# Kernel tuning notes

Measured on AMD Instinct MI355X. Metric: run time of the kernel, lower is better.

Reference implementation:

```python
import jax, jax.numpy as jnp
import numpy as np
from functools import lru_cache


@lru_cache(maxsize=None)
def _mw_basis(L):
    """Fully-normalized associated Legendre basis on MW-style theta grid.

    Returns (Pfull, w):
      Pfull: (L, 2L-1, L) float32, Pfull[l, L-1+m, t] = Nbar_lm * P_l^m(cos theta_t)
             (zero for |m| > l), with Y_lm = Pfull * exp(i m phi).
      w:     (L,) float32 quadrature weights sin(theta)*dtheta*dphi.
    """
    t = np.arange(L)
    theta = np.pi * (2 * t + 1) / (2 * L - 1)  # MW theta samples
    ct, st = np.cos(theta), np.sin(theta)
    P = np.zeros((L, L, L))
    P[0, 0] = np.full(L, np.sqrt(1.0 / (4.0 * np.pi)))
    for m in range(1, L):
        P[m, m] = -np.sqrt((2.0 * m + 1.0) / (2.0 * m)) * st * P[m - 1, m - 1]
    for m in range(L - 1):
        P[m + 1, m] = np.sqrt(2.0 * m + 3.0) * ct * P[m, m]
    for m in range(L):
        for l in range(m + 2, L):
            a = np.sqrt((4.0 * l * l - 1.0) / (l * l - m * m))
            b = np.sqrt(((2.0 * l + 1.0) * (l - 1 - m) * (l - 1 + m)) / ((2.0 * l - 3.0) * (l * l - m * m)))
            P[l, m] = a * ct * P[l - 1, m] - b * P[l - 2, m]
    Pfull = np.zeros((L, 2 * L - 1, L), dtype=np.float32)
    for m in range(L):
        Pfull[:, L - 1 + m, :] = P[:, m, :]
        if m > 0:
            Pfull[:, L - 1 - m, :] = ((-1.0) ** m) * P[:, m, :]
    dang = 2.0 * np.pi / (2 * L - 1)  # theta and phi spacing
    w = (st * dang * dang).astype(np.float32)
    return jnp.asarray(Pfull), jnp.asarray(w)


def sht_forward(x):
    """x: (L, 2L-1, C) real -> flm: (L, 2L-1, C) complex, m indexed -(L-1)..(L-1)."""
    L = x.shape[0]
    P, w = _mw_basis(L)
    F = jnp.fft.fft(x.astype(jnp.complex64), axis=1)           # k = 0..2L-2
    F = jnp.concatenate([F[:, L:, :], F[:, :L, :]], axis=1)     # reorder to m = -(L-1)..L-1
    # flm = sum_t w_t Nbar P_l^m(theta_t) * Fm(theta_t)
    return jnp.einsum('lmt,tmc->lmc', P * w[None, None, :], F)


def sht_inverse(flm):
    """flm: (L, 2L-1, C) complex -> f: (L, 2L-1, C) complex on MW grid."""
    L = flm.shape[0]
    P, _ = _mw_basis(L)
    G = jnp.einsum('lmc,lmt->tmc', flm, P)                      # (theta, m, C)
    G = jnp.concatenate([G[:, L - 1:, :], G[:, :L - 1, :]], axis=1)  # m order -> fft k order
    return jnp.fft.ifft(G, axis=1) * (2 * L - 1)


def zero_pad_flm(flm, L_out):
    L_in = flm.shape[0]
    p = L_out - L_in
    return jnp.pad(flm, ((0, p), (p, p), (0, 0)))


L_IN = 256
L_FREQ = 128
L_OUT = 256
C_IN = 32
C_OUT = 32
T_DIM = 256


def setup_inputs() -> dict:
    key = jax.random.key(0)
    ks = jax.random.split(key, 8)
    return {
        'x': jax.random.normal(ks[0], (L_IN, 2 * L_IN - 1, C_IN), jnp.float32),
        't_emb': jax.random.normal(ks[1], (T_DIM,), jnp.float32),
        'weight_real': 0.02 * jax.random.normal(ks[2], (L_FREQ, C_IN, C_OUT), jnp.float32),
        'weight_imag': 0.02 * jax.random.normal(ks[3], (L_FREQ, C_IN, C_OUT), jnp.float32),
        'w_tr': jax.random.normal(ks[4], (T_DIM, L_FREQ), jnp.float32) / np.sqrt(T_DIM),
        'b_tr': jnp.zeros((L_FREQ,), jnp.float32),
        'w_ti': jax.random.normal(ks[5], (T_DIM, L_FREQ), jnp.float32) / np.sqrt(T_DIM),
        'b_ti': jnp.zeros((L_FREQ,), jnp.float32),
    }


def reference(x, t_emb, weight_real, weight_imag, w_tr, b_tr, w_ti, b_ti):
    # forward SHT over all channels at once
    flm = sht_forward(x)                                       # (L_in, 2L_in-1, C_in) complex64
    # bilinear resize of the spectrum to the used bandlimit (real/imag separately)
    tgt = (L_FREQ, 2 * L_FREQ - 1, flm.shape[2])
    flm = (jax.image.resize(jnp.real(flm), tgt, 'bilinear')
           + 1j * jax.image.resize(jnp.imag(flm), tgt, 'bilinear'))
    # time-modulated per-degree complex spectral weights
    t_cplx = (t_emb @ w_tr + b_tr) + 1j * (t_emb @ w_ti + b_ti)   # (L_freq,)
    weight = t_cplx[:, None, None] * (weight_real + 1j * weight_imag)  # (L_freq, C_in, C_out)
    flm = jnp.einsum('lmi,lio->lmo', flm, weight)
    # zero pad to output bandlimit and inverse SHT
    flm = zero_pad_flm(flm, L_OUT)                             # (L_out, 2L_out-1, C_out)
    x_out = jnp.real(sht_inverse(flm))
    return x_out
```

## Files before the change

### kernel.cpp

```cpp
#include <hip/hip_runtime.h>
#include <math.h>

#define PI_D 3.14159265358979323846

typedef short v8s __attribute__((ext_vector_type(8)));
typedef float v4f __attribute__((ext_vector_type(4)));

constexpr size_t OFF_PA   = 0;
constexpr size_t OFF_PT   = 8388608;
constexpr size_t OFF_SFRE = 12582912;
constexpr size_t OFF_SFIM = 14680064;
constexpr size_t OFF_FRE  = 16777216;
constexpr size_t OFF_FIM  = 18874368;
constexpr size_t OFF_CRE  = 20971520;
constexpr size_t OFF_CIM  = 22016000;
constexpr size_t OFF_AF   = 23060480;
constexpr size_t OFF_AI   = 23191552;
constexpr size_t OFF_WQ   = 23322624;
constexpr size_t OFF_TC   = 23322880;
constexpr size_t OFF_WLW  = 23323136;
constexpr size_t OFF_WLI  = 23323648;
constexpr size_t OFF_WMW  = 23324160;
constexpr size_t OFF_WMI  = 23325696;
constexpr size_t OFF_GRE  = OFF_FRE;
constexpr size_t OFF_GIM  = OFF_FIM;

__device__ __forceinline__ short f2bf(float f) {
  unsigned u = __float_as_uint(f);
  unsigned r = (u + 0x7FFFu + ((u >> 16) & 1u)) >> 16;
  return (short)r;
}

__global__ void k_prep(const float* t_emb, const float* w_tr, const float* b_tr,
                       const float* w_ti, const float* b_ti, float* ws) {
  int bx = blockIdx.x, tid = threadIdx.x;
  if (bx < 2048) {
    int g = bx * 256 + tid;
    bool inv = (g >= 262144);
    int gid = inv ? g - 262144 : g;
    int j = gid & 7, lane = (gid >> 3) & 63, ks = (gid >> 9) & 15, mt = gid >> 13;
    int m = mt * 16 + (lane & 15);
    int k = ks * 32 + ((lane >> 4) << 3) + j;
    float v = 0.f;
    if (!inv) {
      if (k < 511) {
        int mm = (m < 256) ? m : m - 256;
        int kk = (mm * k) % 511;
        float ang = (float)(2.0 * PI_D / 511.0) * (float)kk;
        float s, c; __sincosf(ang, &s, &c);
        v = (m < 256) ? c : -s;
      }
      ((short*)(ws + OFF_AF))[gid] = f2bf(v);
    } else {
      if (m < 511 && k < 510) {
        int jj = (k < 255) ? k : k - 255;
        int jm = jj - 127;
        int kk = ((jm * m) % 511 + 511) % 511;
        float ang = (float)(2.0 * PI_D / 511.0) * (float)kk;
        float s, c; __sincosf(ang, &s, &c);
        v = (k < 255) ? c : -s;
      }
      ((short*)(ws + OFF_AI))[gid] = f2bf(v);
    }
    return;
  }
  if (tid < 256) {
    double theta = PI_D * (2.0 * tid + 1.0) / 511.0;
    double dang = 2.0 * PI_D / 511.0;
    ws[OFF_WQ + tid] = (float)(sin(theta) * dang * dang);
  }
  {
    int h = tid >> 7, o = tid & 127;
    const float* W = h ? w_ti : w_tr;
    float s = h ? b_ti[o] : b_tr[o];
    for (int T = 0; T < 256; ++T) s += t_emb[T] * W[T * 128 + o];
    ws[OFF_TC + h * 128 + o] = s;
  }
  if (tid < 128) {
    double sf = 2.0 * tid + 0.5;
    double wv[4]; int iv[4]; double wsum = 0.0;
    for (int a = 0; a < 4; ++a) {
      int t = 2 * tid - 1 + a;
      double r = 1.0 - fabs(sf - (double)t) * 0.5;
      bool valid = (t >= 0 && t < 256 && r > 0.0);
      wv[a] = valid ? r : 0.0; iv[a] = valid ? t : 0;
      wsum += wv[a];
    }
    for (int a = 0; a < 4; ++a) {
      ws[OFF_WLW + tid * 4 + a] = (float)(wv[a] / wsum);
      ((int*)(ws + OFF_WLI))[tid * 4 + a] = iv[a];
    }
  }
  if (tid < 255) {
    double inv2 = 511.0 / 255.0;
    double sf = (tid + 0.5) * inv2 - 0.5;
    int t0 = (int)floor(sf) - 2;
    double wv[6]; int iv[6]; double wsum = 0.0;
    for (int b = 0; b < 6; ++b) {
      int t = t0 + b;
      double r = 1.0 - fabs(sf - (double)t) * (255.0 / 511.0);
      bool valid = (t >= 0 && t < 511 && r > 0.0);
      wv[b] = valid ? r : 0.0; iv[b] = valid ? t : 0;
      wsum += wv[b];
    }
    for (int b = 0; b < 6; ++b) {
      ws[OFF_WMW + tid * 6 + b] = (float)(wv[b] / wsum);
      ((int*)(ws + OFF_WMI))[tid * 6 + b] = iv[b];
    }
  }
}

__global__ __launch_bounds__(256) void k_legendre(float* ws) {
  int m = blockIdx.x, t = threadIdx.x;
  __shared__ double cA[256], cB[256], cS[256];
  {
    int l = t;
    if (l >= 1) cS[l] = -sqrt((2.0 * l + 1.0) / (2.0 * l));
    if (l >= m + 2) {
      double ll = l, mm = m;
      double den = ll * ll - mm * mm;
      cA[l] = sqrt((4.0 * ll * ll - 1.0) / den);
      cB[l] = sqrt((2.0 * ll + 1.0) * (ll - 1.0 - mm) * (ll - 1.0 + mm) /
                   ((2.0 * ll - 3.0) * den));
    }
  }
  __syncthreads();
  __shared__ short tile[16 * 280];
  __shared__ short tileT[256 * 34];
  bool wantPT = (m < 128);
  short* PAp = (short*)(ws + OFF_PA) + (size_t)m * 65536;
  short* PTp = (short*)(ws + OFF_PT) + (size_t)m * 65536;
  double theta = PI_D * (2.0 * t + 1.0) / 511.0;
  double ct = cos(theta), st = sin(theta);
  double p0 = sqrt(1.0 / (4.0 * PI_D));
  for (int k = 1; k <= m; ++k) p0 *= cS[k] * st;
  double pm1 = 0.0, pcur = 0.0;
  for (int lt = 0; lt < 16; ++lt) {
    for (int li = 0; li < 16; ++li) {
      int l = lt * 16 + li;
      float v;
      if (l < m) v = 0.f;
      else if (l == m) { pcur = p0; v = (float)pcur; }
      else if (l == m + 1) { pm1 = pcur; pcur = sqrt(2.0 * m + 3.0) * ct * pm1; v = (float)pcur; }
      else { double p2 = cA[l] * ct * pcur - cB[l] * pm1; pm1 = pcur; pcur = p2; v = (float)p2; }
      short bv = f2bf(v);
      tile[li * 280 + t] = bv;
      if (wantPT) tileT[t * 34 + li] = bv;
    }
    __syncthreads();
#pragma unroll
    for (int pass = 0; pass < 2; ++pass) {
      int ch = pass * 256 + t;
      int li = ch & 15, T0 = ch >> 4;
      size_t dst = (size_t)lt * 4096 + (size_t)(T0 >> 2) * 512 + (size_t)((T0 & 3) * 16 + li) * 8;
      *(v8s*)(PAp + dst) = *(const v8s*)(tile + li * 280 + T0 * 8);
    }
    if (wantPT) {
#pragma unroll
      for (int pass = 0; pass < 2; ++pass) {
        int ch = pass * 256 + t;
        int tt = ch >> 1, li0 = (ch & 1) * 8;
        size_t dst = (size_t)(tt >> 4) * 4096 + (size_t)(lt >> 1) * 512 +
                     (size_t)(((lt & 1) * 2 + (li0 >> 3)) * 16 + (tt & 15)) * 8;
        const int* src = (const int*)(tileT + tt * 34 + li0);
        int* d = (int*)(PTp + dst);
        d[0] = src[0]; d[1] = src[1]; d[2] = src[2]; d[3] = src[3];
      }
    }
    __syncthreads();
  }
}

__global__ __launch_bounds__(256) void k_gemm_f(const float* x, float* ws) {
  int nt = blockIdx.x, t = blockIdx.y;
  int tid = threadIdx.x, wave = tid >> 6, lane = tid & 63;
  const v8s* A = (const v8s*)(ws + OFF_AF);
  float wq = ws[OFF_WQ + t];
  const float* xb = x + (size_t)t * 511 * 32 + nt * 16 + (lane & 15);
  int phiB = (lane >> 4) << 3;
  int mtB = wave * 8;
  v4f acc[8];
#pragma unroll
  for (int i = 0; i < 8; ++i) acc[i] = (v4f){0.f, 0.f, 0.f, 0.f};
  for (int ks = 0; ks < 16; ++ks) {
    v8s b;
    int phi0 = ks * 32 + phiB;
#pragma unroll
    for (int j = 0; j < 8; ++j) {
      int phi = phi0 + j;
      float v = (phi < 511) ? wq * xb[(size_t)phi * 32] : 0.f;
      b[j] = f2bf(v);
    }
#pragma unroll
    for (int i = 0; i < 8; ++i) {
      v8s a = A[(size_t)((mtB + i) * 16 + ks) * 64 + lane];
      acc[i] = __builtin_amdgcn_mfma_f32_16x16x32_bf16(a, b, acc[i], 0, 0, 0);
    }
  }
  int quad = lane >> 4, cn = nt * 16 + (lane & 15);
#pragma unroll
  for (int i = 0; i < 8; ++i) {
    int mt = mtB + i;
#pragma unroll
    for (int r = 0; r < 4; ++r) {
      int mp = mt * 16 + quad * 4 + r;
      float v = acc[i][r];
      if (mp < 256) ws[OFF_FRE + ((size_t)mp * 256 + t) * 32 + cn] = v;
      else          ws[OFF_FIM + ((size_t)(mp - 256) * 256 + t) * 32 + cn] = v;
    }
  }
}

__global__ __launch_bounds__(512) void k_legfwd(float* ws) {
  int m = blockIdx.x;
  int tid = threadIdx.x, wave = tid >> 6, lane = tid & 63;
  const v8s* A = (const v8s*)(ws + OFF_PA) + (size_t)m * 8192;
  int mt0 = wave * 2;
  int cl = lane & 15, tB = (lane >> 4) << 3;
  v4f acc[2][4];
#pragma unroll
  for (int i = 0; i < 2; ++i)
#pragma unroll
    for (int n = 0; n < 4; ++n) acc[i][n] = (v4f){0.f, 0.f, 0.f, 0.f};
  bool sk0 = (mt0 * 16 + 15) < m;
  bool sk1 = (mt0 * 16 + 31) < m;
  if (!(sk0 && sk1)) {
    for (int ks = 0; ks < 8; ++ks) {
      int t0 = ks * 32 + tB;
      v8s b[4];
#pragma unroll
      for (int n = 0; n < 4; ++n) {
        int cp = n * 16 + cl;
        const float* Fb = ws + (cp < 32 ? OFF_FRE : OFF_FIM) +
                          (size_t)m * 8192 + (size_t)t0 * 32 + (cp & 31);
#pragma unroll
        for (int j = 0; j < 8; ++j) b[n][j] = f2bf(Fb[(size_t)j * 32]);
      }
      if (!sk0) {
        v8s a = A[(size_t)mt0 * 512 + ks * 64 + lane];
        acc[0][0] = __builtin_amdgcn_mfma_f32_16x16x32_bf16(a, b[0], acc[0][0], 0, 0, 0);
        acc[0][1] = __builtin_amdgcn_mfma_f32_16x16x32_bf16(a, b[1], acc[0][1], 0, 0, 0);
        acc[0][2] = __builtin_amdgcn_mfma_f32_16x16x32_bf16(a, b[2], acc[0][2], 0, 0, 0);
        acc[0][3] = __builtin_amdgcn_mfma_f32_16x16x32_bf16(a, b[3], acc[0][3], 0, 0, 0);
      }
      if (!sk1) {
        v8s a = A[(size_t)(mt0 + 1) * 512 + ks * 64 + lane];
        acc[1][0] = __builtin_amdgcn_mfma_f32_16x16x32_bf16(a, b[0], acc[1][0], 0, 0, 0);
        acc[1][1] = __builtin_amdgcn_mfma_f32_16x16x32_bf16(a, b[1], acc[1][1], 0, 0, 0);
        acc[1][2] = __builtin_amdgcn_mfma_f32_16x16x32_bf16(a, b[2], acc[1][2], 0, 0, 0);
        acc[1][3] = __builtin_amdgcn_mfma_f32_16x16x32_bf16(a, b[3], acc[1][3], 0, 0, 0);
      }
    }
  }
  int quad = lane >> 4;
#pragma unroll
  for (int i = 0; i < 2; ++i) {
    bool sk = i ? sk1 : sk0;
#pragma unroll
    for (int n = 0; n < 4; ++n) {
      int cp = n * 16 + cl;
      float* dst = ws + ((cp >= 32) ? OFF_SFIM : OFF_SFRE) + (size_t)m * 8192 + (cp & 31);
#pragma unroll
      for (int r = 0; r < 4; ++r) {
        int l = (mt0 + i) * 16 + quad * 4 + r;
        dst[(size_t)l * 32] = sk ? 0.f : acc[i][n][r];
      }
    }
  }
}

__global__ __launch_bounds__(256) void k_conv(const float* w_real, const float* w_imag, float* ws) {
  int jq = blockIdx.x, l = blockIdx.y;
  int tid = threadIdx.x;
  int jl = tid >> 5, o = tid & 31;
  __shared__ __align__(16) float wr[32 * 36];
  __shared__ __align__(16) float wi[32 * 36];
  __shared__ __align__(16) float fr[8 * 32];
  __shared__ __align__(16) float fi[8 * 32];
  {
    int oo = tid >> 3, i4 = (tid & 7) * 4;
    float tcr = ws[OFF_TC + l], tci = ws[OFF_TC + 128 + l];
#pragma unroll
    for (int q = 0; q < 4; ++q) {
      int i = i4 + q;
      float a = w_real[(size_t)l * 1024 + i * 32 + oo];
      float b = w_imag[(size_t)l * 1024 + i * 32 + oo];
      wr[oo * 36 + i] = tcr * a - tci * b;
      wi[oo * 36 + i] = tcr * b + tci * a;
    }
  }
  const float* SFRE = ws + OFF_SFRE;
  const float* SFIM = ws + OFF_SFIM;
  const float* WMW = ws + OFF_WMW;
  const int* WMI = (const int*)(ws + OFF_WMI);
  float wl[4]; int liv[4];
#pragma unroll
  for (int a = 0; a < 4; ++a) {
    wl[a] = ws[OFF_WLW + l * 4 + a];
    liv[a] = ((const int*)(ws + OFF_WLI))[l * 4 + a];
  }
  for (int ji = 0; ji < 8; ++ji) {
    int j = jq * 64 + ji * 8 + jl;
    int jp = (j < 255) ? j : 254;
    float accr = 0.f, acci = 0.f;
    for (int b = 0; b < 6; ++b) {
      float wm = WMW[jp * 6 + b];
      int jm = WMI[jp * 6 + b];
      bool mneg = (jm < 255);
      int mm = mneg ? (255 - jm) : (jm - 255);
      float fre_f = (mneg && (mm & 1)) ? -1.f : 1.f;
      float fim_f = mneg ? -fre_f : 1.f;
#pragma unroll
      for (int a = 0; a < 4; ++a) {
        float w = wm * wl[a];
        size_t base = ((size_t)mm * 256 + liv[a]) * 32 + o;
        accr = fmaf(w * fre_f, SFRE[base], accr);
        acci = fmaf(w * fim_f, SFIM[base], acci);
      }
    }
    __syncthreads();
    fr[jl * 32 + o] = accr;
    fi[jl * 32 + o] = acci;
    __syncthreads();
    float sr = 0.f, si = 0.f;
#pragma unroll
    for (int i0 = 0; i0 < 32; i0 += 4) {
      float4 f_r = *(const float4*)(fr + jl * 32 + i0);
      float4 f_i = *(const float4*)(fi + jl * 32 + i0);
      float4 w_r = *(const float4*)(wr + o * 36 + i0);
      float4 w_i = *(const float4*)(wi + o * 36 + i0);
      sr += f_r.x * w_r.x - f_i.x * w_i.x;  si += f_r.x * w_i.x + f_i.x * w_r.x;
      sr += f_r.y * w_r.y - f_i.y * w_i.y;  si += f_r.y * w_i.y + f_i.y * w_r.y;
      sr += f_r.z * w_r.z - f_i.z * w_i.z;  si += f_r.z * w_i.z + f_i.z * w_r.z;
      sr += f_r.w * w_r.w - f_i.w * w_i.w;  si += f_r.w * w_i.w + f_i.w * w_r.w;
    }
    if (j < 255) {
      float s = (j < 127 && ((127 - j) & 1)) ? -1.f : 1.f;
      ws[OFF_CRE + ((size_t)j * 128 + l) * 32 + o] = s * sr;
      ws[OFF_CIM + ((size_t)j * 128 + l) * 32 + o] = s * si;
    }
  }
}

__global__ __launch_bounds__(512) void k_gemm_linv(float* ws) {
  int j = blockIdx.x;
  int d = j - 127; int mm = (d < 0) ? -d : d;
  int tid = threadIdx.x, wave = tid >> 6, lane = tid & 63;
  const v8s* A = (const v8s*)(ws + OFF_PT) + (size_t)mm * 8192;
  int mt0 = wave * 2;
  int cl = lane & 15, lB = (lane >> 4) << 3;
  v4f acc[2][4];
#pragma unroll
  for (int i = 0; i < 2; ++i)
#pragma unroll
    for (int n = 0; n < 4; ++n) acc[i][n] = (v4f){0.f, 0.f, 0.f, 0.f};
  int ks0 = mm >> 5;
  for (int ks = ks0; ks < 4; ++ks) {
    int l0 = ks * 32 + lB;
    v8s b[4];
#pragma unroll
    for (int n = 0; n < 4; ++n) {
      int cp = n * 16 + cl;
      const float* Cb = ws + (cp < 32 ? OFF_CRE : OFF_CIM) +
                        ((size_t)j * 128 + l0) * 32 + (cp & 31);
#pragma unroll
      for (int j8 = 0; j8 < 8; ++j8) b[n][j8] = f2bf(Cb[(size_t)j8 * 32]);
    }
    v8s a0 = A[(size_t)mt0 * 512 + ks * 64 + lane];
    v8s a1 = A[(size_t)(mt0 + 1) * 512 + ks * 64 + lane];
    acc[0][0] = __builtin_amdgcn_mfma_f32_16x16x32_bf16(a0, b[0], acc[0][0], 0, 0, 0);
    acc[0][1] = __builtin_amdgcn_mfma_f32_16x16x32_bf16(a0, b[1], acc[0][1], 0, 0, 0);
    acc[0][2] = __builtin_amdgcn_mfma_f32_16x16x32_bf16(a0, b[2], acc[0][2], 0, 0, 0);
    acc[0][3] = __builtin_amdgcn_mfma_f32_16x16x32_bf16(a0, b[3], acc[0][3], 0, 0, 0);
    acc[1][0] = __builtin_amdgcn_mfma_f32_16x16x32_bf16(a1, b[0], acc[1][0], 0, 0, 0);
    acc[1][1] = __builtin_amdgcn_mfma_f32_16x16x32_bf16(a1, b[1], acc[1][1], 0, 0, 0);
    acc[1][2] = __builtin_amdgcn_mfma_f32_16x16x32_bf16(a1, b[2], acc[1][2], 0, 0, 0);
    acc[1][3] = __builtin_amdgcn_mfma_f32_16x16x32_bf16(a1, b[3], acc[1][3], 0, 0, 0);
  }
  int quad = lane >> 4;
#pragma unroll
  for (int i = 0; i < 2; ++i) {
#pragma unroll
    for (int n = 0; n < 4; ++n) {
      int cp = n * 16 + cl;
      float* dst = ws + ((cp >= 32) ? OFF_GIM : OFF_GRE) + (size_t)(cp & 31);
#pragma unroll
      for (int r = 0; r < 4; ++r) {
        int t = (mt0 + i) * 16 + quad * 4 + r;
        dst[((size_t)t * 255 + j) * 32] = acc[i][n][r];
      }
    }
  }
}

__global__ __launch_bounds__(256) void k_gemm_i(const float* ws, float* out) {
  int nt = blockIdx.x, t = blockIdx.y;
  int tid = threadIdx.x, wave = tid >> 6, lane = tid & 63;
  const v8s* A = (const v8s*)(ws + OFF_AI);
  const float* GRE = ws + OFF_GRE;
  const float* GIM = ws + OFF_GIM;
  int mtB = wave * 8;
  int cn = nt * 16 + (lane & 15);
  int kB = (lane >> 4) << 3;
  v4f acc[8];
#pragma unroll
  for (int i = 0; i < 8; ++i) acc[i] = (v4f){0.f, 0.f, 0.f, 0.f};
  for (int ks = 0; ks < 16; ++ks) {
    v8s b;
    int k0 = ks * 32 + kB;
#pragma unroll
    for (int j8 = 0; j8 < 8; ++j8) {
      int k = k0 + j8;
      float v = 0.f;
      if (k < 255)      v = GRE[((size_t)t * 255 + k) * 32 + cn];
      else if (k < 510) v = GIM[((size_t)t * 255 + (k - 255)) * 32 + cn];
      b[j8] = f2bf(v);
    }
#pragma unroll
    for (int i = 0; i < 8; ++i) {
      v8s a = A[(size_t)((mtB + i) * 16 + ks) * 64 + lane];
      acc[i] = __builtin_amdgcn_mfma_f32_16x16x32_bf16(a, b, acc[i], 0, 0, 0);
    }
  }
  int quad = lane >> 4;
#pragma unroll
  for (int i = 0; i < 8; ++i) {
    int mt = mtB + i;
#pragma unroll
    for (int r = 0; r < 4; ++r) {
      int phi = mt * 16 + quad * 4 + r;
      if (phi < 511) out[((size_t)t * 511 + phi) * 32 + cn] = acc[i][r];
    }
  }
}

extern "C" void kernel_launch(void* const* d_in, const int* in_sizes, int n_in,
                              void* d_out, int out_size, void* d_ws, size_t ws_size,
                              hipStream_t stream) {
  const float* x = (const float*)d_in[0];
  const float* t_emb = (const float*)d_in[1];
  const float* w_real = (const float*)d_in[2];
  const float* w_imag = (const float*)d_in[3];
  const float* w_tr = (const float*)d_in[4];
  const float* b_tr = (const float*)d_in[5];
  const float* w_ti = (const float*)d_in[6];
  const float* b_ti = (const float*)d_in[7];
  float* ws = (float*)d_ws;
  float* out = (float*)d_out;
  (void)in_sizes; (void)n_in; (void)out_size; (void)ws_size;

  hipLaunchKernelGGL(k_prep, dim3(2049), dim3(256), 0, stream,
                     t_emb, w_tr, b_tr, w_ti, b_ti, ws);
  hipLaunchKernelGGL(k_legendre, dim3(256), dim3(256), 0, stream, ws);
  hipLaunchKernelGGL(k_gemm_f, dim3(2, 256), dim3(256), 0, stream, x, ws);
  hipLaunchKernelGGL(k_legfwd, dim3(256), dim3(512), 0, stream, ws);
  hipLaunchKernelGGL(k_conv, dim3(4, 128), dim3(256), 0, stream, w_real, w_imag, ws);
  hipLaunchKernelGGL(k_gemm_linv, dim3(255), dim3(512), 0, stream, ws);
  hipLaunchKernelGGL(k_gemm_i, dim3(2, 256), dim3(256), 0, stream, ws, out);
}
```

Before: 230.0 us.

## Split GEMM tiles across more waves and register-prefetch B operands

The four MFMA GEMM kernels now give each wave fewer output tiles: the phi/k GEMMs use twice as many blocks, and the Legendre GEMMs use 1024-thread blocks with one M-tile per wave. Each kernel also software-pipelines the strided B-operand loads, reading the next k-slice into registers while MFMAs run on the current one. The aim is more parallelism and latency hiding for the global loads. In exchange, the shared B loads are repeated across more waves and blocks, and register pressure rises with 1024-thread blocks.

```diff
diff --git a/kernel.cpp b/kernel.cpp
--- a/kernel.cpp
+++ b/kernel.cpp
@@ -172,34 +172,49 @@
 }
 
 __global__ __launch_bounds__(256) void k_gemm_f(const float* x, float* ws) {
-  int nt = blockIdx.x, t = blockIdx.y;
+  int bx = blockIdx.x, t = blockIdx.y;
+  int nt = bx & 1, mh = bx >> 1;
   int tid = threadIdx.x, wave = tid >> 6, lane = tid & 63;
   const v8s* A = (const v8s*)(ws + OFF_AF);
   float wq = ws[OFF_WQ + t];
   const float* xb = x + (size_t)t * 511 * 32 + nt * 16 + (lane & 15);
   int phiB = (lane >> 4) << 3;
-  int mtB = wave * 8;
-  v4f acc[8];
-#pragma unroll
-  for (int i = 0; i < 8; ++i) acc[i] = (v4f){0.f, 0.f, 0.f, 0.f};
+  int mtB = mh * 16 + wave * 4;
+  v4f acc[4];
+#pragma unroll
+  for (int i = 0; i < 4; ++i) acc[i] = (v4f){0.f, 0.f, 0.f, 0.f};
+  float bv[8];
+#pragma unroll
+  for (int j = 0; j < 8; ++j) {
+    int phi = phiB + j;
+    bv[j] = (phi < 511) ? xb[(size_t)phi * 32] : 0.f;
+  }
   for (int ks = 0; ks < 16; ++ks) {
+    float bn[8];
+    if (ks < 15) {
+      int phi0 = (ks + 1) * 32 + phiB;
+#pragma unroll
+      for (int j = 0; j < 8; ++j) {
+        int phi = phi0 + j;
+        bn[j] = (phi < 511) ? xb[(size_t)phi * 32] : 0.f;
+      }
+    }
     v8s b;
-    int phi0 = ks * 32 + phiB;
-#pragma unroll
-    for (int j = 0; j < 8; ++j) {
-      int phi = phi0 + j;
-      float v = (phi < 511) ? wq * xb[(size_t)phi * 32] : 0.f;
-      b[j] = f2bf(v);
-    }
-#pragma unroll
-    for (int i = 0; i < 8; ++i) {
+#pragma unroll
+    for (int j = 0; j < 8; ++j) b[j] = f2bf(wq * bv[j]);
+#pragma unroll
+    for (int i = 0; i < 4; ++i) {
       v8s a = A[(size_t)((mtB + i) * 16 + ks) * 64 + lane];
       acc[i] = __builtin_amdgcn_mfma_f32_16x16x32_bf16(a, b, acc[i], 0, 0, 0);
     }
+    if (ks < 15) {
+#pragma unroll
+      for (int j = 0; j < 8; ++j) bv[j] = bn[j];
+    }
   }
   int quad = lane >> 4, cn = nt * 16 + (lane & 15);
 #pragma unroll
-  for (int i = 0; i < 8; ++i) {
+  for (int i = 0; i < 4; ++i) {
     int mt = mtB + i;
 #pragma unroll
     for (int r = 0; r < 4; ++r) {
@@ -211,60 +226,60 @@
   }
 }
 
-__global__ __launch_bounds__(512) void k_legfwd(float* ws) {
+__global__ __launch_bounds__(1024) void k_legfwd(float* ws) {
   int m = blockIdx.x;
-  int tid = threadIdx.x, wave = tid >> 6, lane = tid & 63;
+  int tid = threadIdx.x, mt = tid >> 6, lane = tid & 63;
   const v8s* A = (const v8s*)(ws + OFF_PA) + (size_t)m * 8192;
-  int mt0 = wave * 2;
   int cl = lane & 15, tB = (lane >> 4) << 3;
-  v4f acc[2][4];
-#pragma unroll
-  for (int i = 0; i < 2; ++i)
-#pragma unroll
-    for (int n = 0; n < 4; ++n) acc[i][n] = (v4f){0.f, 0.f, 0.f, 0.f};
-  bool sk0 = (mt0 * 16 + 15) < m;
-  bool sk1 = (mt0 * 16 + 31) < m;
-  if (!(sk0 && sk1)) {
-    for (int ks = 0; ks < 8; ++ks) {
-      int t0 = ks * 32 + tB;
-      v8s b[4];
-#pragma unroll
-      for (int n = 0; n < 4; ++n) {
-        int cp = n * 16 + cl;
-        const float* Fb = ws + (cp < 32 ? OFF_FRE : OFF_FIM) +
-                          (size_t)m * 8192 + (size_t)t0 * 32 + (cp & 31);
-#pragma unroll
-        for (int j = 0; j < 8; ++j) b[n][j] = f2bf(Fb[(size_t)j * 32]);
-      }
-      if (!sk0) {
-        v8s a = A[(size_t)mt0 * 512 + ks * 64 + lane];
-        acc[0][0] = __builtin_amdgcn_mfma_f32_16x16x32_bf16(a, b[0], acc[0][0], 0, 0, 0);
-        acc[0][1] = __builtin_amdgcn_mfma_f32_16x16x32_bf16(a, b[1], acc[0][1], 0, 0, 0);
-        acc[0][2] = __builtin_amdgcn_mfma_f32_16x16x32_bf16(a, b[2], acc[0][2], 0, 0, 0);
-        acc[0][3] = __builtin_amdgcn_mfma_f32_16x16x32_bf16(a, b[3], acc[0][3], 0, 0, 0);
-      }
-      if (!sk1) {
-        v8s a = A[(size_t)(mt0 + 1) * 512 + ks * 64 + lane];
-        acc[1][0] = __builtin_amdgcn_mfma_f32_16x16x32_bf16(a, b[0], acc[1][0], 0, 0, 0);
-        acc[1][1] = __builtin_amdgcn_mfma_f32_16x16x32_bf16(a, b[1], acc[1][1], 0, 0, 0);
-        acc[1][2] = __builtin_amdgcn_mfma_f32_16x16x32_bf16(a, b[2], acc[1][2], 0, 0, 0);
-        acc[1][3] = __builtin_amdgcn_mfma_f32_16x16x32_bf16(a, b[3], acc[1][3], 0, 0, 0);
-      }
-    }
-  }
   int quad = lane >> 4;
-#pragma unroll
-  for (int i = 0; i < 2; ++i) {
-    bool sk = i ? sk1 : sk0;
+  v4f acc[4];
+#pragma unroll
+  for (int n = 0; n < 4; ++n) acc[n] = (v4f){0.f, 0.f, 0.f, 0.f};
+  bool sk = (mt * 16 + 15) < m;
+  if (!sk) {
+    const float* Fb[4];
 #pragma unroll
     for (int n = 0; n < 4; ++n) {
       int cp = n * 16 + cl;
-      float* dst = ws + ((cp >= 32) ? OFF_SFIM : OFF_SFRE) + (size_t)m * 8192 + (cp & 31);
-#pragma unroll
-      for (int r = 0; r < 4; ++r) {
-        int l = (mt0 + i) * 16 + quad * 4 + r;
-        dst[(size_t)l * 32] = sk ? 0.f : acc[i][n][r];
-      }
+      Fb[n] = ws + (cp < 32 ? OFF_FRE : OFF_FIM) + (size_t)m * 8192 + (size_t)tB * 32 + (cp & 31);
+    }
+    float bv[4][8];
+#pragma unroll
+    for (int n = 0; n < 4; ++n)
+#pragma unroll
+      for (int j = 0; j < 8; ++j) bv[n][j] = Fb[n][(size_t)j * 32];
+    for (int ks = 0; ks < 8; ++ks) {
+      float bn[4][8];
+      if (ks < 7) {
+#pragma unroll
+        for (int n = 0; n < 4; ++n)
+#pragma unroll
+          for (int j = 0; j < 8; ++j) bn[n][j] = Fb[n][(size_t)((ks + 1) * 32 + j) * 32];
+      }
+      v8s a = A[(size_t)mt * 512 + ks * 64 + lane];
+#pragma unroll
+      for (int n = 0; n < 4; ++n) {
+        v8s b;
+#pragma unroll
+        for (int j = 0; j < 8; ++j) b[j] = f2bf(bv[n][j]);
+        acc[n] = __builtin_amdgcn_mfma_f32_16x16x32_bf16(a, b, acc[n], 0, 0, 0);
+      }
+      if (ks < 7) {
+#pragma unroll
+        for (int n = 0; n < 4; ++n)
+#pragma unroll
+          for (int j = 0; j < 8; ++j) bv[n][j] = bn[n][j];
+      }
+    }
+  }
+#pragma unroll
+  for (int n = 0; n < 4; ++n) {
+    int cp = n * 16 + cl;
+    float* dst = ws + ((cp >= 32) ? OFF_SFIM : OFF_SFRE) + (size_t)m * 8192 + (cp & 31);
+#pragma unroll
+    for (int r = 0; r < 4; ++r) {
+      int l = mt * 16 + quad * 4 + r;
+      dst[(size_t)l * 32] = sk ? 0.f : acc[n][r];
     }
   }
 }
@@ -342,89 +357,114 @@
   }
 }
 
-__global__ __launch_bounds__(512) void k_gemm_linv(float* ws) {
+__global__ __launch_bounds__(1024) void k_gemm_linv(float* ws) {
   int j = blockIdx.x;
   int d = j - 127; int mm = (d < 0) ? -d : d;
-  int tid = threadIdx.x, wave = tid >> 6, lane = tid & 63;
+  int tid = threadIdx.x, mt = tid >> 6, lane = tid & 63;
   const v8s* A = (const v8s*)(ws + OFF_PT) + (size_t)mm * 8192;
-  int mt0 = wave * 2;
   int cl = lane & 15, lB = (lane >> 4) << 3;
-  v4f acc[2][4];
-#pragma unroll
-  for (int i = 0; i < 2; ++i)
-#pragma unroll
-    for (int n = 0; n < 4; ++n) acc[i][n] = (v4f){0.f, 0.f, 0.f, 0.f};
+  int quad = lane >> 4;
+  v4f acc[4];
+#pragma unroll
+  for (int n = 0; n < 4; ++n) acc[n] = (v4f){0.f, 0.f, 0.f, 0.f};
   int ks0 = mm >> 5;
+  const float* Cb[4];
+#pragma unroll
+  for (int n = 0; n < 4; ++n) {
+    int cp = n * 16 + cl;
+    Cb[n] = ws + (cp < 32 ? OFF_CRE : OFF_CIM) + ((size_t)j * 128 + lB) * 32 + (cp & 31);
+  }
+  float bv[4][8];
+#pragma unroll
+  for (int n = 0; n < 4; ++n)
+#pragma unroll
+    for (int j8 = 0; j8 < 8; ++j8) bv[n][j8] = Cb[n][(size_t)(ks0 * 32 + j8) * 32];
   for (int ks = ks0; ks < 4; ++ks) {
-    int l0 = ks * 32 + lB;
-    v8s b[4];
+    float bn[4][8];
+    if (ks < 3) {
+#pragma unroll
+      for (int n = 0; n < 4; ++n)
+#pragma unroll
+        for (int j8 = 0; j8 < 8; ++j8) bn[n][j8] = Cb[n][(size_t)((ks + 1) * 32 + j8) * 32];
+    }
+    v8s a = A[(size_t)mt * 512 + ks * 64 + lane];
 #pragma unroll
     for (int n = 0; n < 4; ++n) {
-      int cp = n * 16 + cl;
-      const float* Cb = ws + (cp < 32 ? OFF_CRE : OFF_CIM) +
-                        ((size_t)j * 128 + l0) * 32 + (cp & 31);
-#pragma unroll
-      for (int j8 = 0; j8 < 8; ++j8) b[n][j8] = f2bf(Cb[(size_t)j8 * 32]);
-    }
-    v8s a0 = A[(size_t)mt0 * 512 + ks * 64 + lane];
-    v8s a1 = A[(size_t)(mt0 + 1) * 512 + ks * 64 + lane];
-    acc[0][0] = __builtin_amdgcn_mfma_f32_16x16x32_bf16(a0, b[0], acc[0][0], 0, 0, 0);
-    acc[0][1] = __builtin_amdgcn_mfma_f32_16x16x32_bf16(a0, b[1], acc[0][1], 0, 0, 0);
-    acc[0][2] = __builtin_amdgcn_mfma_f32_16x16x32_bf16(a0, b[2], acc[0][2], 0, 0, 0);
-    acc[0][3] = __builtin_amdgcn_mfma_f32_16x16x32_bf16(a0, b[3], acc[0][3], 0, 0, 0);
-    acc[1][0] = __builtin_amdgcn_mfma_f32_16x16x32_bf16(a1, b[0], acc[1][0], 0, 0, 0);
-    acc[1][1] = __builtin_amdgcn_mfma_f32_16x16x32_bf16(a1, b[1], acc[1][1], 0, 0, 0);
-    acc[1][2] = __builtin_amdgcn_mfma_f32_16x16x32_bf16(a1, b[2], acc[1][2], 0, 0, 0);
-    acc[1][3] = __builtin_amdgcn_mfma_f32_16x16x32_bf16(a1, b[3], acc[1][3], 0, 0, 0);
-  }
-  int quad = lane >> 4;
-#pragma unroll
-  for (int i = 0; i < 2; ++i) {
-#pragma unroll
-    for (int n = 0; n < 4; ++n) {
-      int cp = n * 16 + cl;
-      float* dst = ws + ((cp >= 32) ? OFF_GIM : OFF_GRE) + (size_t)(cp & 31);
-#pragma unroll
-      for (int r = 0; r < 4; ++r) {
-        int t = (mt0 + i) * 16 + quad * 4 + r;
-        dst[((size_t)t * 255 + j) * 32] = acc[i][n][r];
-      }
+      v8s b;
+#pragma unroll
+      for (int j8 = 0; j8 < 8; ++j8) b[j8] = f2bf(bv[n][j8]);
+      acc[n] = __builtin_amdgcn_mfma_f32_16x16x32_bf16(a, b, acc[n], 0, 0, 0);
+    }
+    if (ks < 3) {
+#pragma unroll
+      for (int n = 0; n < 4; ++n)
+#pragma unroll
+        for (int j8 = 0; j8 < 8; ++j8) bv[n][j8] = bn[n][j8];
+    }
+  }
+#pragma unroll
+  for (int n = 0; n < 4; ++n) {
+    int cp = n * 16 + cl;
+    float* dst = ws + ((cp >= 32) ? OFF_GIM : OFF_GRE) + (size_t)(cp & 31);
+#pragma unroll
+    for (int r = 0; r < 4; ++r) {
+      int t = mt * 16 + quad * 4 + r;
+      dst[((size_t)t * 255 + j) * 32] = acc[n][r];
     }
   }
 }
 
 __global__ __launch_bounds__(256) void k_gemm_i(const float* ws, float* out) {
-  int nt = blockIdx.x, t = blockIdx.y;
+  int bx = blockIdx.x, t = blockIdx.y;
+  int nt = bx & 1, mh = bx >> 1;
   int tid = threadIdx.x, wave = tid >> 6, lane = tid & 63;
   const v8s* A = (const v8s*)(ws + OFF_AI);
   const float* GRE = ws + OFF_GRE;
   const float* GIM = ws + OFF_GIM;
-  int mtB = wave * 8;
+  int mtB = mh * 16 + wave * 4;
   int cn = nt * 16 + (lane & 15);
   int kB = (lane >> 4) << 3;
-  v4f acc[8];
-#pragma unroll
-  for (int i = 0; i < 8; ++i) acc[i] = (v4f){0.f, 0.f, 0.f, 0.f};
+  v4f acc[4];
+#pragma unroll
+  for (int i = 0; i < 4; ++i) acc[i] = (v4f){0.f, 0.f, 0.f, 0.f};
+  float bv[8];
+#pragma unroll
+  for (int j8 = 0; j8 < 8; ++j8) {
+    int k = kB + j8;
+    float v = 0.f;
+    if (k < 255)      v = GRE[((size_t)t * 255 + k) * 32 + cn];
+    else if (k < 510) v = GIM[((size_t)t * 255 + (k - 255)) * 32 + cn];
+    bv[j8] = v;
+  }
   for (int ks = 0; ks < 16; ++ks) {
+    float bn[8];
+    if (ks < 15) {
+      int k0 = (ks + 1) * 32 + kB;
+#pragma unroll
+      for (int j8 = 0; j8 < 8; ++j8) {
+        int k = k0 + j8;
+        float v = 0.f;
+        if (k < 255)      v = GRE[((size_t)t * 255 + k) * 32 + cn];
+        else if (k < 510) v = GIM[((size_t)t * 255 + (k - 255)) * 32 + cn];
+        bn[j8] = v;
+      }
+    }
     v8s b;
-    int k0 = ks * 32 + kB;
-#pragma unroll
-    for (int j8 = 0; j8 < 8; ++j8) {
-      int k = k0 + j8;
-      float v = 0.f;
-      if (k < 255)      v = GRE[((size_t)t * 255 + k) * 32 + cn];
-      else if (k < 510) v = GIM[((size_t)t * 255 + (k - 255)) * 32 + cn];
-      b[j8] = f2bf(v);
-    }
-#pragma unroll
-    for (int i = 0; i < 8; ++i) {
+#pragma unroll
+    for (int j8 = 0; j8 < 8; ++j8) b[j8] = f2bf(bv[j8]);
+#pragma unroll
+    for (int i = 0; i < 4; ++i) {
       v8s a = A[(size_t)((mtB + i) * 16 + ks) * 64 + lane];
       acc[i] = __builtin_amdgcn_mfma_f32_16x16x32_bf16(a, b, acc[i], 0, 0, 0);
     }
+    if (ks < 15) {
+#pragma unroll
+      for (int j8 = 0; j8 < 8; ++j8) bv[j8] = bn[j8];
+    }
   }
   int quad = lane >> 4;
 #pragma unroll
-  for (int i = 0; i < 8; ++i) {
+  for (int i = 0; i < 4; ++i) {
     int mt = mtB + i;
 #pragma unroll
     for (int r = 0; r < 4; ++r) {
@@ -452,9 +492,9 @@
   hipLaunchKernelGGL(k_prep, dim3(2049), dim3(256), 0, stream,
                      t_emb, w_tr, b_tr, w_ti, b_ti, ws);
   hipLaunchKernelGGL(k_legendre, dim3(256), dim3(256), 0, stream, ws);
-  hipLaunchKernelGGL(k_gemm_f, dim3(2, 256), dim3(256), 0, stream, x, ws);
-  hipLaunchKernelGGL(k_legfwd, dim3(256), dim3(512), 0, stream, ws);
+  hipLaunchKernelGGL(k_gemm_f, dim3(4, 256), dim3(256), 0, stream, x, ws);
+  hipLaunchKernelGGL(k_legfwd, dim3(256), dim3(1024), 0, stream, ws);
   hipLaunchKernelGGL(k_conv, dim3(4, 128), dim3(256), 0, stream, w_real, w_imag, ws);
-  hipLaunchKernelGGL(k_gemm_linv, dim3(255), dim3(512), 0, stream, ws);
-  hipLaunchKernelGGL(k_gemm_i, dim3(2, 256), dim3(256), 0, stream, ws, out);
-}
+  hipLaunchKernelGGL(k_gemm_linv, dim3(255), dim3(1024), 0, stream, ws);
+  hipLaunchKernelGGL(k_gemm_i, dim3(4, 256), dim3(256), 0, stream, ws, out);
+}
```

Result: faster. 223.2 us (-3.0%).
